# Performance work log

Measured on AMD Instinct MI355X. Metric: run time of the kernel, lower is better.

Reference implementation:

```python
import jax, jax.numpy as jnp
import numpy as np

NUM_GROUP = 16
LN_EPS = 1e-5


def setup_inputs() -> dict:
    key = jax.random.key(0)
    ks = jax.random.split(key, 3)
    B, N, C = 8, 4096, 1024
    x = jax.random.normal(ks[0], (B, N, C), dtype=jnp.float32)
    Wqkv = jax.random.normal(ks[1], (C, 3 * C), dtype=jnp.float32) * (C ** -0.5)
    Wproj = jax.random.normal(ks[2], (C, C), dtype=jnp.float32) * (C ** -0.5)
    bproj = jnp.zeros((C,), dtype=jnp.float32)
    gamma = jnp.ones((C,), dtype=jnp.float32)
    beta = jnp.zeros((C,), dtype=jnp.float32)
    return {"x": x, "Wqkv": Wqkv, "Wproj": Wproj, "bproj": bproj,
            "gamma": gamma, "beta": beta}


def reference(x, Wqkv, Wproj, bproj, gamma, beta):
    B, N, C = x.shape
    G = NUM_GROUP
    hd = C // G
    scale = hd ** -0.5
    # QKV projection: [B,N,3,G,hd]
    qkv = (x @ Wqkv).reshape(B, N, 3, G, hd)
    q = jnp.transpose(qkv[:, :, 0], (0, 2, 1, 3))  # [B,G,N,hd]
    k = jnp.transpose(qkv[:, :, 1], (0, 2, 1, 3)) * scale
    v = jnp.transpose(qkv[:, :, 2], (0, 2, 1, 3))
    # transposed (channel) attention: k^T @ v -> [B,G,hd,hd]
    attn = jnp.einsum('bgnd,bgne->bgde', k, v)
    attn = jax.nn.softmax(attn, axis=-1)
    # (attn @ q^T)^T : out[b,g,n,d] = sum_e attn[b,g,d,e] * q[b,g,n,e]
    out = jnp.einsum('bgde,bgne->bgnd', attn, q)  # [B,G,N,hd]
    out = jnp.transpose(out, (0, 2, 1, 3)).reshape(B, N, C)
    out = out @ Wproj + bproj  # dropout is identity in eval mode
    h = x + out
    # LayerNorm over last dim
    mu = jnp.mean(h, axis=-1, keepdims=True)
    var = jnp.var(h, axis=-1, keepdims=True)
    return gamma * (h - mu) * jax.lax.rsqrt(var + LN_EPS) + beta
```

## Files before the change

kernel.cpp:

```cpp
#include <hip/hip_runtime.h>
#include <cstdint>

typedef __bf16 bf16;
typedef __bf16 bf16x8 __attribute__((ext_vector_type(8)));
typedef float f32x4 __attribute__((ext_vector_type(4)));

#define DEVI __device__ __forceinline__

DEVI float bits2f(uint32_t u){ union{uint32_t u;float f;}x; x.u=u; return x.f; }

DEVI void gload_lds16(const void* g, void* l){
  __builtin_amdgcn_global_load_lds(
    (const __attribute__((address_space(1))) uint32_t*)g,
    (__attribute__((address_space(3))) uint32_t*)l, 16, 0, 0);
}

__global__ __launch_bounds__(256) void k_cast(const float* __restrict__ x, bf16* __restrict__ o, int n){
  int i = (blockIdx.x*256 + threadIdx.x)*8;
  if (i >= n) return;
  float4 a = *(const float4*)(x+i);
  float4 b = *(const float4*)(x+i+4);
  union { bf16 h[8]; uint4 u; } r;
  r.h[0]=(bf16)a.x; r.h[1]=(bf16)a.y; r.h[2]=(bf16)a.z; r.h[3]=(bf16)a.w;
  r.h[4]=(bf16)b.x; r.h[5]=(bf16)b.y; r.h[6]=(bf16)b.z; r.h[7]=(bf16)b.w;
  *(uint4*)(o+i) = r.u;
}

__global__ __launch_bounds__(256) void k_castT(const float* __restrict__ x, bf16* __restrict__ xb,
                                               bf16* __restrict__ xT){
  const int b = blockIdx.z;
  x  += (size_t)b*4194304; xb += (size_t)b*4194304; xT += (size_t)b*4194304;
  const int n0 = blockIdx.y*64, c0 = blockIdx.x*64;
  __shared__ float sF[64][65];
  const int t = threadIdx.x;
  const int lr = t>>4, lc4 = (t&15)*4;
  #pragma unroll
  for (int i=0;i<4;++i){
    int r = lr + i*16;
    float4 v = *(const float4*)(x + (size_t)(n0+r)*1024 + c0 + lc4);
    sF[r][lc4+0]=v.x; sF[r][lc4+1]=v.y; sF[r][lc4+2]=v.z; sF[r][lc4+3]=v.w;
  }
  __syncthreads();
  const int wr = t>>3, wc8 = (t&7)*8;
  #pragma unroll
  for (int i=0;i<2;++i){
    int r = wr + i*32;
    union{ bf16 h[8]; uint4 u; } p;
    #pragma unroll
    for (int j=0;j<8;++j) p.h[j] = (bf16)sF[r][wc8+j];
    *(uint4*)(xb + (size_t)(n0+r)*1024 + c0 + wc8) = p.u;
  }
  #pragma unroll
  for (int i=0;i<2;++i){
    int c = wr + i*32;
    union{ bf16 h[8]; uint4 u; } p;
    #pragma unroll
    for (int j=0;j<8;++j) p.h[j] = (bf16)sF[wc8+j][c];
    *(uint4*)(xT + (size_t)(c0+c)*4096 + n0 + wc8) = p.u;
  }
}

__global__ __launch_bounds__(256) void k_transpose(const float* __restrict__ W, bf16* __restrict__ WT,
                                                   int R, int Ccols){
  __shared__ float tile[32][33];
  int bc = blockIdx.x*32, br = blockIdx.y*32;
  int lc = threadIdx.x & 31, lr = threadIdx.x >> 5;
  #pragma unroll
  for (int i=0;i<4;i++){
    int r = lr + i*8;
    tile[r][lc] = W[(size_t)(br+r)*Ccols + bc + lc];
  }
  __syncthreads();
  #pragma unroll
  for (int i=0;i<4;i++){
    int r = lr + i*8;
    WT[(size_t)(bc+r)*R + br + lc] = (bf16)tile[lc][r];
  }
}

__global__ __launch_bounds__(256) void k_gemm128(
    const bf16* __restrict__ A, const bf16* __restrict__ BT, bf16* __restrict__ C,
    int N, int K, int lda, int ldb,
    size_t As, size_t Bs, size_t Cs)
{
  A += blockIdx.z*As; BT += blockIdx.z*Bs; C += blockIdx.z*Cs;
  __shared__ __align__(16) bf16 sA[128*64];
  __shared__ __align__(16) bf16 sB[128*64];
  const int t = threadIdx.x, w = t>>6, l = t&63;
  const int bm = blockIdx.y*128, bn = blockIdx.x*128;
  const int wr = (w>>1)*64, wc = (w&1)*64;
  f32x4 acc[4][4] = {};
  const int srow = l>>3;
  const int scol = ((l&7) ^ (l>>3))*8;
  const int nk = K>>6;
  for (int kt=0; kt<nk; ++kt) {
    const int k0 = kt*64;
    #pragma unroll
    for (int i=0;i<4;++i){
      int c = w*4+i;
      int row = c*8 + srow;
      gload_lds16(A  + (size_t)(bm+row)*lda + k0 + scol, (char*)sA + c*1024);
      gload_lds16(BT + (size_t)(bn+row)*ldb + k0 + scol, (char*)sB + c*1024);
    }
    __syncthreads();
    #pragma unroll
    for (int kk=0; kk<64; kk+=32) {
      bf16x8 af[4], bfr[4];
      const int xr = ((kk + 8*(l>>4))*2) ^ ((l&7)<<4);
      #pragma unroll
      for (int mf=0;mf<4;++mf){
        int row = wr + mf*16 + (l&15);
        af[mf] = *(const bf16x8*)((const char*)sA + row*128 + xr);
      }
      #pragma unroll
      for (int nf=0;nf<4;++nf){
        int row = wc + nf*16 + (l&15);
        bfr[nf] = *(const bf16x8*)((const char*)sB + row*128 + xr);
      }
      #pragma unroll
      for (int mf=0;mf<4;++mf)
        #pragma unroll
        for (int nf=0;nf<4;++nf)
          acc[mf][nf] = __builtin_amdgcn_mfma_f32_16x16x32_bf16(af[mf], bfr[nf], acc[mf][nf], 0,0,0);
    }
    __syncthreads();
  }
  #pragma unroll
  for (int mf=0;mf<4;++mf)
    #pragma unroll
    for (int nf=0;nf<4;++nf)
      #pragma unroll
      for (int r=0;r<4;++r){
        int row = bm + wr + mf*16 + (l>>4)*4 + r;
        int col = bn + wc + nf*16 + (l&15);
        C[(size_t)row*N + col] = (bf16)acc[mf][nf][r];
      }
}

__global__ __launch_bounds__(512, 2) void k_gemm256(
    const bf16* __restrict__ A, const bf16* __restrict__ BT, bf16* __restrict__ C,
    int N, int K,
    const float* __restrict__ bias, const bf16* __restrict__ resid,
    size_t As, size_t Bs, size_t Cs, size_t Rs)
{
  A += blockIdx.z*As; BT += blockIdx.z*Bs; C += blockIdx.z*Cs; resid += blockIdx.z*Rs;
  __shared__ __align__(16) bf16 lds[2][2][256*64];
  bf16* bA0 = &lds[0][0][0]; bf16* bB0 = &lds[0][1][0];
  bf16* bA1 = &lds[1][0][0]; bf16* bB1 = &lds[1][1][0];

  const int t = threadIdx.x, w = t>>6, l = t&63;
  const int wm = w>>2, wn = w&3;

  const int nwg = gridDim.x * gridDim.y;
  const int orig = blockIdx.y * gridDim.x + blockIdx.x;
  const int q = nwg >> 3, r = nwg & 7;
  const int xcd = orig & 7, loc = orig >> 3;
  const int swz = (xcd < r ? xcd*(q+1) : r*(q+1) + (xcd-r)*q) + loc;
  const int bx = swz % gridDim.x, by = swz / gridDim.x;
  const int bm = by*256, bn = bx*256;

  const int co0 = (16*(l>>4)) ^ ((l&7)<<4);
  const int co1 = (64 + 16*(l>>4)) ^ ((l&7)<<4);

  auto stageA = [&](const bf16* G, bf16* Ldst, int j, int k0){
    int row = wm*128 + wn*32 + j*8 + (l>>3);
    int col = 8*((l&7) ^ (l>>3));
    gload_lds16(G + (size_t)(bm + row)*K + k0 + col,
                Ldst + (wm*128 + wn*32 + j*8)*64);
  };
  auto stageB = [&](const bf16* G, bf16* Ldst, int j, int k0){
    int row = j*64 + w*8 + (l>>3);
    int col = 8*((l&7) ^ (l>>3));
    gload_lds16(G + (size_t)(bn + row)*K + k0 + col,
                Ldst + (j*64 + w*8)*64);
  };

#define RD_AA(dst, qd, base) {                                                  \
    const int r0 = wm*128 + (qd)*32 + (l&15);                                   \
    dst[0][0] = *(const bf16x8*)((const char*)(base) + (r0   )*128 + co0);      \
    dst[0][1] = *(const bf16x8*)((const char*)(base) + (r0   )*128 + co1);      \
    dst[1][0] = *(const bf16x8*)((const char*)(base) + (r0+16)*128 + co0);      \
    dst[1][1] = *(const bf16x8*)((const char*)(base) + (r0+16)*128 + co1);      \
  }

#define MFMA_Q(P, AA) {                                                         \
    __builtin_amdgcn_s_setprio(1);                                              \
    _Pragma("unroll")                                                           \
    for (int kk=0;kk<2;++kk)                                                    \
      _Pragma("unroll")                                                         \
      for (int i=0;i<2;++i)                                                     \
        _Pragma("unroll")                                                       \
        for (int nf=0;nf<4;++nf)                                                \
          acc[2*(P)+i][nf] = __builtin_amdgcn_mfma_f32_16x16x32_bf16(           \
              AA[i][kk], bfr[nf][kk], acc[2*(P)+i][nf], 0,0,0);                 \
    __builtin_amdgcn_s_setprio(0);                                              \
  }

#define BAR asm volatile("s_barrier" ::: "memory")

  f32x4 acc[8][4] = {};
  const int NT = K >> 6;

  #pragma unroll
  for (int j=0;j<4;++j) stageA(A, bA0, j, 0);
  #pragma unroll
  for (int j=0;j<4;++j) stageB(BT, bB0, j, 0);
  __builtin_amdgcn_sched_barrier(0);
  if (NT > 1){
    #pragma unroll
    for (int j=0;j<4;++j) stageB(BT, bB1, j, 64);
    asm volatile("s_waitcnt vmcnt(4)" ::: "memory");
  } else {
    asm volatile("s_waitcnt vmcnt(0)" ::: "memory");
  }
  BAR;

  bf16x8 aaA[2][2], aaB[2][2];
  RD_AA(aaA, wn, bA0);

  for (int T = 0; T < NT; ++T){
    bf16* sA  = (T&1) ? bA1 : bA0;
    bf16* sB  = (T&1) ? bB1 : bB0;
    bf16* sAn = (T&1) ? bA0 : bA1;
    const int kA = (T+1)<<6, kB = (T+2)<<6;
    const bool stA = (T+1) < NT, stB = (T+2) < NT;

    bf16x8 bfr[4][2];
    const int rb = wn*64 + (l&15);
    #pragma unroll
    for (int nf=0;nf<4;++nf){
      bfr[nf][0] = *(const bf16x8*)((const char*)sB + (rb+nf*16)*128 + co0);
      bfr[nf][1] = *(const bf16x8*)((const char*)sB + (rb+nf*16)*128 + co1);
    }

    RD_AA(aaB, (wn+1)&3, sA);
    if (stA){ stageA(A, sAn, 0, kA); stageA(A, sAn, 1, kA); }
    BAR; MFMA_Q(0, aaA); BAR;

    RD_AA(aaA, (wn+2)&3, sA);
    if (stA){ stageA(A, sAn, 2, kA); stageA(A, sAn, 3, kA); }
    BAR; MFMA_Q(1, aaB); BAR;

    RD_AA(aaB, (wn+3)&3, sA);
    if (stB){ stageB(BT, sB, 0, kB); stageB(BT, sB, 1, kB); }
    BAR; MFMA_Q(2, aaA); BAR;

    if (stB){
      stageB(BT, sB, 2, kB); stageB(BT, sB, 3, kB);
      asm volatile("s_waitcnt vmcnt(4)" ::: "memory");
    } else {
      asm volatile("s_waitcnt vmcnt(0)" ::: "memory");
    }
    if (stA) RD_AA(aaA, wn, sAn);
    BAR; MFMA_Q(3, aaB); BAR;
  }
#undef RD_AA
#undef MFMA_Q
#undef BAR

  #pragma unroll
  for (int P=0; P<4; ++P){
    const int qd = (P+wn)&3;
    #pragma unroll
    for (int i=0;i<2;++i){
      #pragma unroll
      for (int nf=0; nf<4; ++nf){
        #pragma unroll
        for (int r2=0; r2<4; ++r2){
          int row = bm + wm*128 + qd*32 + i*16 + (l>>4)*4 + r2;
          int col = bn + wn*64 + nf*16 + (l&15);
          float v = acc[2*P+i][nf][r2] + bias[col] + (float)resid[(size_t)row*N + col];
          C[(size_t)row*N + col] = (bf16)v;
        }
      }
    }
  }
}

__global__ __launch_bounds__(256) void k_sgemm64(const bf16* __restrict__ T2, const bf16* __restrict__ WqkvT,
                                                 bf16* __restrict__ Aatt){
  const int bg = blockIdx.x, b = bg>>4, g = bg&15;
  const bf16* Arows = T2 + (size_t)b*1048576 + (size_t)(g*64)*1024;
  const bf16* Brows = WqkvT + (size_t)(2048 + g*64)*1024;
  __shared__ __align__(16) bf16 sA[64*64];
  __shared__ __align__(16) bf16 sB[64*64];
  const int t = threadIdx.x, w = t>>6, l = t&63;
  const int srow = l>>3, scol = ((l&7)^(l>>3))*8;
  f32x4 acc[4] = {};
  for (int kt=0; kt<16; ++kt){
    const int k0 = kt*64;
    gload_lds16(Arows + (size_t)(w*8+srow)*1024 + k0 + scol,      sA + (w*8)*64);
    gload_lds16(Arows + (size_t)(32+w*8+srow)*1024 + k0 + scol,   sA + (32+w*8)*64);
    gload_lds16(Brows + (size_t)(w*8+srow)*1024 + k0 + scol,      sB + (w*8)*64);
    gload_lds16(Brows + (size_t)(32+w*8+srow)*1024 + k0 + scol,   sB + (32+w*8)*64);
    __syncthreads();
    #pragma unroll
    for (int kk=0; kk<64; kk+=32){
      const int xr = ((kk + 8*(l>>4))*2) ^ ((l&7)<<4);
      bf16x8 af = *(const bf16x8*)((const char*)sA + (w*16+(l&15))*128 + xr);
      #pragma unroll
      for (int nf=0; nf<4; ++nf){
        bf16x8 bfv = *(const bf16x8*)((const char*)sB + (nf*16+(l&15))*128 + xr);
        acc[nf] = __builtin_amdgcn_mfma_f32_16x16x32_bf16(af, bfv, acc[nf], 0,0,0);
      }
    }
    __syncthreads();
  }
  #pragma unroll
  for (int reg=0; reg<4; ++reg){
    float m = -3.4e38f;
    #pragma unroll
    for (int nf=0; nf<4; ++nf) m = fmaxf(m, acc[nf][reg]);
    m = fmaxf(m, __shfl_xor(m,1)); m = fmaxf(m, __shfl_xor(m,2));
    m = fmaxf(m, __shfl_xor(m,4)); m = fmaxf(m, __shfl_xor(m,8));
    float e[4]; float s = 0.f;
    #pragma unroll
    for (int nf=0; nf<4; ++nf){ e[nf] = __expf((acc[nf][reg]-m)*0.125f); s += e[nf]; }
    s += __shfl_xor(s,1); s += __shfl_xor(s,2); s += __shfl_xor(s,4); s += __shfl_xor(s,8);
    const float inv = 1.0f/s;
    const int row = w*16 + (l>>4)*4 + reg;
    #pragma unroll
    for (int nf=0; nf<4; ++nf)
      Aatt[(size_t)bg*4096 + row*64 + nf*16 + (l&15)] = (bf16)(e[nf]*inv);
  }
}

__global__ __launch_bounds__(256) void k_applyW(const bf16* __restrict__ Wqkvb, const bf16* __restrict__ Aatt,
                                                bf16* __restrict__ U){
  const int bg = blockIdx.y, b = bg>>4, g = bg&15;
  const int m0 = blockIdx.x*128;
  __shared__ __align__(16) bf16 Pl[64][72];
  const int t = threadIdx.x, w = t>>6, l = t&63;
  for (int idx=t; idx<1024; idx+=256){
    int r2 = idx>>4, c4 = (idx&15)*4;
    *(uint2*)&Pl[r2][c4] = *(const uint2*)&Aatt[(size_t)bg*4096 + r2*64 + c4];
  }
  __syncthreads();
  f32x4 acc[2][4] = {};
  const bf16* Ab = Wqkvb + (size_t)(m0 + w*32)*3072 + g*64;
  #pragma unroll
  for (int kk=0; kk<64; kk+=32){
    bf16x8 af[2], pf[4];
    #pragma unroll
    for (int mf=0;mf<2;++mf)
      af[mf] = *(const bf16x8*)(Ab + (size_t)(mf*16 + (l&15))*3072 + kk + 8*(l>>4));
    #pragma unroll
    for (int nf=0;nf<4;++nf)
      pf[nf] = *(const bf16x8*)&Pl[nf*16 + (l&15)][kk + 8*(l>>4)];
    #pragma unroll
    for (int mf=0;mf<2;++mf)
      #pragma unroll
      for (int nf=0;nf<4;++nf)
        acc[mf][nf] = __builtin_amdgcn_mfma_f32_16x16x32_bf16(af[mf], pf[nf], acc[mf][nf], 0,0,0);
  }
  #pragma unroll
  for (int mf=0;mf<2;++mf)
    #pragma unroll
    for (int nf=0;nf<4;++nf)
      #pragma unroll
      for (int r=0;r<4;++r){
        int rowc = m0 + w*32 + mf*16 + (l>>4)*4 + r;
        int col = g*64 + nf*16 + (l&15);
        U[(size_t)b*1048576 + (size_t)rowc*1024 + col] = (bf16)acc[mf][nf][r];
      }
}

__global__ __launch_bounds__(256) void k_ln(const bf16* __restrict__ h, const float* __restrict__ gamma,
                                            const float* __restrict__ beta, float* __restrict__ y){
  const int w = threadIdx.x>>6, l = threadIdx.x&63;
  const size_t row = (size_t)blockIdx.x*4 + w;
  const bf16* hr = h + row*1024 + l*16;
  uint4 p0 = *(const uint4*)hr;
  uint4 p1 = *(const uint4*)(hr+8);
  float v[16];
  const uint32_t* pw = (const uint32_t*)&p0;
  #pragma unroll
  for (int i=0;i<4;++i){ v[2*i] = bits2f(pw[i]<<16); v[2*i+1] = bits2f(pw[i]&0xffff0000u); }
  const uint32_t* pw1 = (const uint32_t*)&p1;
  #pragma unroll
  for (int i=0;i<4;++i){ v[8+2*i] = bits2f(pw1[i]<<16); v[8+2*i+1] = bits2f(pw1[i]&0xffff0000u); }
  float s=0.f, s2=0.f;
  #pragma unroll
  for (int i=0;i<16;++i){ s+=v[i]; s2+=v[i]*v[i]; }
  #pragma unroll
  for (int off=1; off<64; off<<=1){ s += __shfl_xor(s,off); s2 += __shfl_xor(s2,off); }
  float mu = s*(1.0f/1024.0f);
  float var = s2*(1.0f/1024.0f) - mu*mu;
  float rinv = rsqrtf(var + 1e-5f);
  const float* gp = gamma + l*16; const float* bp = beta + l*16;
  float o[16];
  #pragma unroll
  for (int i=0;i<16;++i) o[i] = gp[i]*(v[i]-mu)*rinv + bp[i];
  float* yr = y + row*1024 + l*16;
  #pragma unroll
  for (int i=0;i<4;++i) ((float4*)yr)[i] = *(float4*)&o[4*i];
}

extern "C" void kernel_launch(void* const* d_in, const int* in_sizes, int n_in,
                              void* d_out, int out_size, void* d_ws, size_t ws_size,
                              hipStream_t stream){
  const float* x     = (const float*)d_in[0];
  const float* Wqkv  = (const float*)d_in[1];
  const float* Wproj = (const float*)d_in[2];
  const float* bproj = (const float*)d_in[3];
  const float* gamma = (const float*)d_in[4];
  const float* beta  = (const float*)d_in[5];
  float* y = (float*)d_out;

  char* ws = (char*)d_ws;
  size_t off = 0;
  auto alloc = [&](size_t bytes)->void*{ void* p = ws + off; off += (bytes + 255) & ~(size_t)255; return p; };
  bf16* xb     = (bf16*)alloc((size_t)32768*1024*2);
  bf16* xT     = (bf16*)alloc((size_t)8*1024*4096*2);
  bf16* Wqkvb  = (bf16*)alloc((size_t)1024*3072*2);
  bf16* WqkvT  = (bf16*)alloc((size_t)3072*1024*2);
  bf16* WprojT = (bf16*)alloc((size_t)1024*1024*2);
  bf16* Gram   = (bf16*)alloc((size_t)8*1024*1024*2);
  bf16* T2     = (bf16*)alloc((size_t)8*1024*1024*2);
  bf16* Aatt   = (bf16*)alloc((size_t)128*64*64*2);
  bf16* U      = (bf16*)alloc((size_t)8*1024*1024*2);
  bf16* WeffT  = (bf16*)alloc((size_t)8*1024*1024*2);
  bf16* h      = xT;

  const size_t MB1 = 1048576;

  k_castT<<<dim3(16,64,8),256,0,stream>>>(x, xb, xT);
  k_cast<<<1536,256,0,stream>>>(Wqkv, Wqkvb, 3145728);
  k_transpose<<<dim3(96,32),256,0,stream>>>(Wqkv, WqkvT, 1024, 3072);
  k_transpose<<<dim3(32,32),256,0,stream>>>(Wproj, WprojT, 1024, 1024);
  k_gemm128<<<dim3(8,8,8),256,0,stream>>>(xT, xT, Gram, 1024, 4096, 4096, 4096,
                                          (size_t)1024*4096, (size_t)1024*4096, MB1);
  k_gemm128<<<dim3(8,8,8),256,0,stream>>>(WqkvT + (size_t)1024*1024, Gram, T2, 1024, 1024, 1024, 1024,
                                          0, MB1, MB1);
  k_sgemm64<<<128,256,0,stream>>>(T2, WqkvT, Aatt);
  k_applyW<<<dim3(8,128),256,0,stream>>>(Wqkvb, Aatt, U);
  k_gemm128<<<dim3(8,8,8),256,0,stream>>>(WprojT, U, WeffT, 1024, 1024, 1024, 1024,
                                          0, MB1, MB1);
  k_gemm256<<<dim3(4,16,8),512,0,stream>>>(xb, WeffT, h, 1024, 1024, bproj, xb,
                                           (size_t)4096*1024, MB1, (size_t)4096*1024, (size_t)4096*1024);
  k_ln<<<8192,256,0,stream>>>(h, gamma, beta, y);
}
```

Before: 350.5 us.

## Exploit Gram matrix symmetry to compute only upper-triangular tiles

```diff
diff --git a/kernel.cpp b/kernel.cpp
--- a/kernel.cpp
+++ b/kernel.cpp
@@ -8,6 +8,9 @@
 #define DEVI __device__ __forceinline__
 
 DEVI float bits2f(uint32_t u){ union{uint32_t u;float f;}x; x.u=u; return x.f; }
+DEVI uint32_t packbf2(float a, float b){
+  union{ bf16 h[2]; uint32_t u; } p; p.h[0]=(bf16)a; p.h[1]=(bf16)b; return p.u;
+}
 
 DEVI void gload_lds16(const void* g, void* l){
   __builtin_amdgcn_global_load_lds(
@@ -137,6 +140,90 @@
       }
 }
 
+__global__ __launch_bounds__(256) void k_gramsym(const bf16* __restrict__ xT, bf16* __restrict__ Gram){
+  const int d = blockIdx.y*36 + blockIdx.x;
+  const int vt = (d & 7)*36 + (d >> 3);
+  const int b = vt/36;
+  int t36 = vt - b*36;
+  int i = 0;
+  while (t36 >= 8 - i){ t36 -= 8 - i; ++i; }
+  const int j = i + t36;
+  const bf16* A = xT + (size_t)b*4194304;
+  bf16* C = Gram + (size_t)b*1048576;
+  const int bm = i*128, bn = j*128;
+
+  __shared__ __align__(16) bf16 sAB[16384];
+  bf16* sA = sAB; bf16* sB = sAB + 8192;
+  const int t = threadIdx.x, w = t>>6, l = t&63;
+  const int wr = (w>>1)*64, wc = (w&1)*64;
+  f32x4 acc[4][4] = {};
+  const int srow = l>>3;
+  const int scol = ((l&7) ^ (l>>3))*8;
+  for (int kt=0; kt<64; ++kt) {
+    const int k0 = kt*64;
+    #pragma unroll
+    for (int ii=0;ii<4;++ii){
+      int c = w*4+ii;
+      int row = c*8 + srow;
+      gload_lds16(A + (size_t)(bm+row)*4096 + k0 + scol, (char*)sA + c*1024);
+      gload_lds16(A + (size_t)(bn+row)*4096 + k0 + scol, (char*)sB + c*1024);
+    }
+    __syncthreads();
+    #pragma unroll
+    for (int kk=0; kk<64; kk+=32) {
+      bf16x8 af[4], bfr[4];
+      const int xr = ((kk + 8*(l>>4))*2) ^ ((l&7)<<4);
+      #pragma unroll
+      for (int mf=0;mf<4;++mf)
+        af[mf] = *(const bf16x8*)((const char*)sA + (wr+mf*16+(l&15))*128 + xr);
+      #pragma unroll
+      for (int nf=0;nf<4;++nf)
+        bfr[nf] = *(const bf16x8*)((const char*)sB + (wc+nf*16+(l&15))*128 + xr);
+      #pragma unroll
+      for (int mf=0;mf<4;++mf)
+        #pragma unroll
+        for (int nf=0;nf<4;++nf)
+          acc[mf][nf] = __builtin_amdgcn_mfma_f32_16x16x32_bf16(af[mf], bfr[nf], acc[mf][nf], 0,0,0);
+    }
+    __syncthreads();
+  }
+  #pragma unroll
+  for (int mf=0;mf<4;++mf)
+    #pragma unroll
+    for (int nf=0;nf<4;++nf)
+      #pragma unroll
+      for (int r=0;r<4;++r){
+        int row = bm + wr + mf*16 + (l>>4)*4 + r;
+        int col = bn + wc + nf*16 + (l&15);
+        C[(size_t)row*1024 + col] = (bf16)acc[mf][nf][r];
+      }
+  if (i == j) return;
+  for (int h2=0; h2<2; ++h2){
+    __syncthreads();
+    if ((w&1) == h2){
+      #pragma unroll
+      for (int mf=0;mf<4;++mf)
+        #pragma unroll
+        for (int nf=0;nf<4;++nf)
+          #pragma unroll
+          for (int p=0;p<2;++p){
+            int col_local = nf*16 + (l&15);
+            int rowb = wr + mf*16 + (l>>4)*4 + 2*p;
+            *(uint32_t*)((char*)sAB + (col_local*136 + rowb)*2) =
+              packbf2(acc[mf][nf][2*p], acc[mf][nf][2*p+1]);
+          }
+    }
+    __syncthreads();
+    {
+      int col_local = t>>2, sub = t&3;
+      const uint4* src = (const uint4*)((const char*)sAB + col_local*272 + sub*64);
+      uint4 v0 = src[0], v1 = src[1], v2 = src[2], v3 = src[3];
+      bf16* dst = C + (size_t)(bn + h2*64 + col_local)*1024 + bm + sub*32;
+      ((uint4*)dst)[0]=v0; ((uint4*)dst)[1]=v1; ((uint4*)dst)[2]=v2; ((uint4*)dst)[3]=v3;
+    }
+  }
+}
+
 __global__ __launch_bounds__(512, 2) void k_gemm256(
     const bf16* __restrict__ A, const bf16* __restrict__ BT, bf16* __restrict__ C,
     int N, int K,
@@ -428,8 +515,7 @@
   k_cast<<<1536,256,0,stream>>>(Wqkv, Wqkvb, 3145728);
   k_transpose<<<dim3(96,32),256,0,stream>>>(Wqkv, WqkvT, 1024, 3072);
   k_transpose<<<dim3(32,32),256,0,stream>>>(Wproj, WprojT, 1024, 1024);
-  k_gemm128<<<dim3(8,8,8),256,0,stream>>>(xT, xT, Gram, 1024, 4096, 4096, 4096,
-                                          (size_t)1024*4096, (size_t)1024*4096, MB1);
+  k_gramsym<<<dim3(36,8),256,0,stream>>>(xT, Gram);
   k_gemm128<<<dim3(8,8,8),256,0,stream>>>(WqkvT + (size_t)1024*1024, Gram, T2, 1024, 1024, 1024, 1024,
                                           0, MB1, MB1);
   k_sgemm64<<<128,256,0,stream>>>(T2, WqkvT, Aatt);
```

New measurement: 333.4 us. 1.05x faster.

## Exploit Gram symmetry and replace 256-tile projection GEMM with templated 128 GEMM

Applied to the files above, without the earlier changes.

```diff
diff --git a/kernel.cpp b/kernel.cpp
--- a/kernel.cpp
+++ b/kernel.cpp
@@ -8,6 +8,9 @@
 #define DEVI __device__ __forceinline__
 
 DEVI float bits2f(uint32_t u){ union{uint32_t u;float f;}x; x.u=u; return x.f; }
+DEVI uint32_t packbf2(float a, float b){
+  union{ bf16 h[2]; uint32_t u; } p; p.h[0]=(bf16)a; p.h[1]=(bf16)b; return p.u;
+}
 
 DEVI void gload_lds16(const void* g, void* l){
   __builtin_amdgcn_global_load_lds(
@@ -78,12 +81,15 @@
   }
 }
 
+template<int EPI>
 __global__ __launch_bounds__(256) void k_gemm128(
     const bf16* __restrict__ A, const bf16* __restrict__ BT, bf16* __restrict__ C,
     int N, int K, int lda, int ldb,
-    size_t As, size_t Bs, size_t Cs)
+    size_t As, size_t Bs, size_t Cs,
+    const float* __restrict__ bias, const bf16* __restrict__ resid, size_t Rs)
 {
   A += blockIdx.z*As; BT += blockIdx.z*Bs; C += blockIdx.z*Cs;
+  if (EPI==1) resid += blockIdx.z*Rs;
   __shared__ __align__(16) bf16 sA[128*64];
   __shared__ __align__(16) bf16 sB[128*64];
   const int t = threadIdx.x, w = t>>6, l = t&63;
@@ -133,146 +139,90 @@
       for (int r=0;r<4;++r){
         int row = bm + wr + mf*16 + (l>>4)*4 + r;
         int col = bn + wc + nf*16 + (l&15);
-        C[(size_t)row*N + col] = (bf16)acc[mf][nf][r];
-      }
-}
-
-__global__ __launch_bounds__(512, 2) void k_gemm256(
-    const bf16* __restrict__ A, const bf16* __restrict__ BT, bf16* __restrict__ C,
-    int N, int K,
-    const float* __restrict__ bias, const bf16* __restrict__ resid,
-    size_t As, size_t Bs, size_t Cs, size_t Rs)
-{
-  A += blockIdx.z*As; BT += blockIdx.z*Bs; C += blockIdx.z*Cs; resid += blockIdx.z*Rs;
-  __shared__ __align__(16) bf16 lds[2][2][256*64];
-  bf16* bA0 = &lds[0][0][0]; bf16* bB0 = &lds[0][1][0];
-  bf16* bA1 = &lds[1][0][0]; bf16* bB1 = &lds[1][1][0];
-
+        float v = acc[mf][nf][r];
+        if (EPI==1) v += bias[col] + (float)resid[(size_t)row*N + col];
+        C[(size_t)row*N + col] = (bf16)v;
+      }
+}
+
+__global__ __launch_bounds__(512) void k_gramsym(const bf16* __restrict__ xT, bf16* __restrict__ Gram){
+  const int t36o = blockIdx.x, b = blockIdx.y;
+  int t36 = t36o;
+  int i = 0;
+  while (t36 >= 8 - i){ t36 -= 8 - i; ++i; }
+  const int j = i + t36;
+  const bf16* A = xT + (size_t)b*4194304;
+  bf16* C = Gram + (size_t)b*1048576;
+  const int bm = i*128, bn = j*128;
+
+  __shared__ __align__(16) bf16 sAB[16384];
+  bf16* sA = sAB; bf16* sB = sAB + 8192;
   const int t = threadIdx.x, w = t>>6, l = t&63;
-  const int wm = w>>2, wn = w&3;
-
-  const int nwg = gridDim.x * gridDim.y;
-  const int orig = blockIdx.y * gridDim.x + blockIdx.x;
-  const int q = nwg >> 3, r = nwg & 7;
-  const int xcd = orig & 7, loc = orig >> 3;
-  const int swz = (xcd < r ? xcd*(q+1) : r*(q+1) + (xcd-r)*q) + loc;
-  const int bx = swz % gridDim.x, by = swz / gridDim.x;
-  const int bm = by*256, bn = bx*256;
-
-  const int co0 = (16*(l>>4)) ^ ((l&7)<<4);
-  const int co1 = (64 + 16*(l>>4)) ^ ((l&7)<<4);
-
-  auto stageA = [&](const bf16* G, bf16* Ldst, int j, int k0){
-    int row = wm*128 + wn*32 + j*8 + (l>>3);
-    int col = 8*((l&7) ^ (l>>3));
-    gload_lds16(G + (size_t)(bm + row)*K + k0 + col,
-                Ldst + (wm*128 + wn*32 + j*8)*64);
-  };
-  auto stageB = [&](const bf16* G, bf16* Ldst, int j, int k0){
-    int row = j*64 + w*8 + (l>>3);
-    int col = 8*((l&7) ^ (l>>3));
-    gload_lds16(G + (size_t)(bn + row)*K + k0 + col,
-                Ldst + (j*64 + w*8)*64);
-  };
-
-#define RD_AA(dst, qd, base) {                                                  \
-    const int r0 = wm*128 + (qd)*32 + (l&15);                                   \
-    dst[0][0] = *(const bf16x8*)((const char*)(base) + (r0   )*128 + co0);      \
-    dst[0][1] = *(const bf16x8*)((const char*)(base) + (r0   )*128 + co1);      \
-    dst[1][0] = *(const bf16x8*)((const char*)(base) + (r0+16)*128 + co0);      \
-    dst[1][1] = *(const bf16x8*)((const char*)(base) + (r0+16)*128 + co1);      \
-  }
-
-#define MFMA_Q(P, AA) {                                                         \
-    __builtin_amdgcn_s_setprio(1);                                              \
-    _Pragma("unroll")                                                           \
-    for (int kk=0;kk<2;++kk)                                                    \
-      _Pragma("unroll")                                                         \
-      for (int i=0;i<2;++i)                                                     \
-        _Pragma("unroll")                                                       \
-        for (int nf=0;nf<4;++nf)                                                \
-          acc[2*(P)+i][nf] = __builtin_amdgcn_mfma_f32_16x16x32_bf16(           \
-              AA[i][kk], bfr[nf][kk], acc[2*(P)+i][nf], 0,0,0);                 \
-    __builtin_amdgcn_s_setprio(0);                                              \
-  }
-
-#define BAR asm volatile("s_barrier" ::: "memory")
-
-  f32x4 acc[8][4] = {};
-  const int NT = K >> 6;
-
-  #pragma unroll
-  for (int j=0;j<4;++j) stageA(A, bA0, j, 0);
-  #pragma unroll
-  for (int j=0;j<4;++j) stageB(BT, bB0, j, 0);
-  __builtin_amdgcn_sched_barrier(0);
-  if (NT > 1){
-    #pragma unroll
-    for (int j=0;j<4;++j) stageB(BT, bB1, j, 64);
-    asm volatile("s_waitcnt vmcnt(4)" ::: "memory");
-  } else {
-    asm volatile("s_waitcnt vmcnt(0)" ::: "memory");
-  }
-  BAR;
-
-  bf16x8 aaA[2][2], aaB[2][2];
-  RD_AA(aaA, wn, bA0);
-
-  for (int T = 0; T < NT; ++T){
-    bf16* sA  = (T&1) ? bA1 : bA0;
-    bf16* sB  = (T&1) ? bB1 : bB0;
-    bf16* sAn = (T&1) ? bA0 : bA1;
-    const int kA = (T+1)<<6, kB = (T+2)<<6;
-    const bool stA = (T+1) < NT, stB = (T+2) < NT;
-
-    bf16x8 bfr[4][2];
-    const int rb = wn*64 + (l&15);
-    #pragma unroll
-    for (int nf=0;nf<4;++nf){
-      bfr[nf][0] = *(const bf16x8*)((const char*)sB + (rb+nf*16)*128 + co0);
-      bfr[nf][1] = *(const bf16x8*)((const char*)sB + (rb+nf*16)*128 + co1);
-    }
-
-    RD_AA(aaB, (wn+1)&3, sA);
-    if (stA){ stageA(A, sAn, 0, kA); stageA(A, sAn, 1, kA); }
-    BAR; MFMA_Q(0, aaA); BAR;
-
-    RD_AA(aaA, (wn+2)&3, sA);
-    if (stA){ stageA(A, sAn, 2, kA); stageA(A, sAn, 3, kA); }
-    BAR; MFMA_Q(1, aaB); BAR;
-
-    RD_AA(aaB, (wn+3)&3, sA);
-    if (stB){ stageB(BT, sB, 0, kB); stageB(BT, sB, 1, kB); }
-    BAR; MFMA_Q(2, aaA); BAR;
-
-    if (stB){
-      stageB(BT, sB, 2, kB); stageB(BT, sB, 3, kB);
-      asm volatile("s_waitcnt vmcnt(4)" ::: "memory");
-    } else {
-      asm volatile("s_waitcnt vmcnt(0)" ::: "memory");
-    }
-    if (stA) RD_AA(aaA, wn, sAn);
-    BAR; MFMA_Q(3, aaB); BAR;
-  }
-#undef RD_AA
-#undef MFMA_Q
-#undef BAR
-
-  #pragma unroll
-  for (int P=0; P<4; ++P){
-    const int qd = (P+wn)&3;
-    #pragma unroll
-    for (int i=0;i<2;++i){
-      #pragma unroll
-      for (int nf=0; nf<4; ++nf){
+  const int wm = w>>1, wn = w&1;
+  f32x4 acc[2][4] = {};
+  const int srow = l>>3;
+  const int scol = ((l&7) ^ (l>>3))*8;
+  for (int kt=0; kt<64; ++kt) {
+    const int k0 = kt*64;
+    #pragma unroll
+    for (int ii=0;ii<2;++ii){
+      int c = w*2+ii;
+      int row = c*8 + srow;
+      gload_lds16(A + (size_t)(bm+row)*4096 + k0 + scol, (char*)sA + c*1024);
+      gload_lds16(A + (size_t)(bn+row)*4096 + k0 + scol, (char*)sB + c*1024);
+    }
+    __syncthreads();
+    #pragma unroll
+    for (int kk=0; kk<64; kk+=32) {
+      bf16x8 af[2], bfr[4];
+      const int xr = ((kk + 8*(l>>4))*2) ^ ((l&7)<<4);
+      #pragma unroll
+      for (int mf=0;mf<2;++mf)
+        af[mf] = *(const bf16x8*)((const char*)sA + (wm*32+mf*16+(l&15))*128 + xr);
+      #pragma unroll
+      for (int nf=0;nf<4;++nf)
+        bfr[nf] = *(const bf16x8*)((const char*)sB + (wn*64+nf*16+(l&15))*128 + xr);
+      #pragma unroll
+      for (int mf=0;mf<2;++mf)
         #pragma unroll
-        for (int r2=0; r2<4; ++r2){
-          int row = bm + wm*128 + qd*32 + i*16 + (l>>4)*4 + r2;
-          int col = bn + wn*64 + nf*16 + (l&15);
-          float v = acc[2*P+i][nf][r2] + bias[col] + (float)resid[(size_t)row*N + col];
-          C[(size_t)row*N + col] = (bf16)v;
-        }
-      }
+        for (int nf=0;nf<4;++nf)
+          acc[mf][nf] = __builtin_amdgcn_mfma_f32_16x16x32_bf16(af[mf], bfr[nf], acc[mf][nf], 0,0,0);
+    }
+    __syncthreads();
+  }
+  #pragma unroll
+  for (int mf=0;mf<2;++mf)
+    #pragma unroll
+    for (int nf=0;nf<4;++nf)
+      #pragma unroll
+      for (int r=0;r<4;++r){
+        int row = bm + wm*32 + mf*16 + (l>>4)*4 + r;
+        int col = bn + wn*64 + nf*16 + (l&15);
+        C[(size_t)row*1024 + col] = (bf16)acc[mf][nf][r];
+      }
+  if (i == j) return;
+  for (int h2=0; h2<2; ++h2){
+    __syncthreads();
+    if (wn == h2){
+      #pragma unroll
+      for (int mf=0;mf<2;++mf)
+        #pragma unroll
+        for (int nf=0;nf<4;++nf)
+          #pragma unroll
+          for (int p=0;p<2;++p){
+            int col_local = nf*16 + (l&15);
+            int rowb = wm*32 + mf*16 + (l>>4)*4 + 2*p;
+            *(uint32_t*)((char*)sAB + (col_local*136 + rowb)*2) =
+              packbf2(acc[mf][nf][2*p], acc[mf][nf][2*p+1]);
+          }
+    }
+    __syncthreads();
+    {
+      int col_local = t>>3, sub = t&7;
+      const uint4* src = (const uint4*)((const char*)sAB + col_local*272 + sub*32);
+      uint4 v0 = src[0], v1 = src[1];
+      bf16* dst = C + (size_t)(bn + h2*64 + col_local)*1024 + bm + sub*16;
+      ((uint4*)dst)[0]=v0; ((uint4*)dst)[1]=v1;
     }
   }
 }
@@ -423,20 +373,20 @@
   bf16* h      = xT;
 
   const size_t MB1 = 1048576;
+  const size_t MB4 = (size_t)4096*1024;
 
   k_castT<<<dim3(16,64,8),256,0,stream>>>(x, xb, xT);
   k_cast<<<1536,256,0,stream>>>(Wqkv, Wqkvb, 3145728);
   k_transpose<<<dim3(96,32),256,0,stream>>>(Wqkv, WqkvT, 1024, 3072);
   k_transpose<<<dim3(32,32),256,0,stream>>>(Wproj, WprojT, 1024, 1024);
-  k_gemm128<<<dim3(8,8,8),256,0,stream>>>(xT, xT, Gram, 1024, 4096, 4096, 4096,
-                                          (size_t)1024*4096, (size_t)1024*4096, MB1);
-  k_gemm128<<<dim3(8,8,8),256,0,stream>>>(WqkvT + (size_t)1024*1024, Gram, T2, 1024, 1024, 1024, 1024,
-                                          0, MB1, MB1);
+  k_gramsym<<<dim3(36,8),512,0,stream>>>(xT, Gram);
+  k_gemm128<0><<<dim3(8,8,8),256,0,stream>>>(WqkvT + (size_t)1024*1024, Gram, T2, 1024, 1024, 1024, 1024,
+                                             0, MB1, MB1, nullptr, nullptr, 0);
   k_sgemm64<<<128,256,0,stream>>>(T2, WqkvT, Aatt);
   k_applyW<<<dim3(8,128),256,0,stream>>>(Wqkvb, Aatt, U);
-  k_gemm128<<<dim3(8,8,8),256,0,stream>>>(WprojT, U, WeffT, 1024, 1024, 1024, 1024,
-                                          0, MB1, MB1);
-  k_gemm256<<<dim3(4,16,8),512,0,stream>>>(xb, WeffT, h, 1024, 1024, bproj, xb,
-                                           (size_t)4096*1024, MB1, (size_t)4096*1024, (size_t)4096*1024);
+  k_gemm128<0><<<dim3(8,8,8),256,0,stream>>>(WprojT, U, WeffT, 1024, 1024, 1024, 1024,
+                                             0, MB1, MB1, nullptr, nullptr, 0);
+  k_gemm128<1><<<dim3(8,32,8),256,0,stream>>>(xb, WeffT, h, 1024, 1024, 1024, 1024,
+                                              MB4, MB1, MB4, bproj, xb, MB4);
   k_ln<<<8192,256,0,stream>>>(h, gamma, beta, y);
 }
```

After: 365.4 us. 4.3% more time.
